# Kernel tuning notes

Hardware: AMD Instinct MI355X
Metric: run time of the kernel (lower is better)

Reference implementation:

```python
import jax, jax.numpy as jnp
import numpy as np

Q_DIM = 32
HID = 512
OFF = Q_DIM * (Q_DIM - 1) // 2  # 496 strictly-lower-triangular entries


def setup_inputs() -> dict:
    key = jax.random.key(0)
    ks = jax.random.split(key, 20)

    def w(k, shape, fan_in):
        return (jax.random.normal(k, shape, jnp.float32) / np.float32(np.sqrt(fan_in)))

    return {
        "q": jax.random.normal(ks[0], (1, Q_DIM), jnp.float32),
        "q_t": jax.random.normal(ks[1], (1, Q_DIM), jnp.float32),
        "q_tt": jax.random.normal(ks[2], (1, Q_DIM), jnp.float32),
        # L-network (torch Linear convention: y = x @ W.T + b)
        "W1": w(ks[3], (HID, Q_DIM), Q_DIM), "b1": jnp.zeros((HID,), jnp.float32),
        "W2": w(ks[4], (HID, HID), HID),     "b2": jnp.zeros((HID,), jnp.float32),
        "W3": w(ks[5], (HID, HID), HID),     "b3": jnp.zeros((HID,), jnp.float32),
        "Wd": w(ks[6], (Q_DIM, HID), HID),   "bd": jnp.zeros((Q_DIM,), jnp.float32),
        "Wo": w(ks[7], (OFF, HID), HID),     "bo": jnp.zeros((OFF,), jnp.float32),
        # g-network
        "Wg1": w(ks[8], (HID, Q_DIM), Q_DIM), "bg1": jnp.zeros((HID,), jnp.float32),
        "Wg2": w(ks[9], (HID, HID), HID),     "bg2": jnp.zeros((HID,), jnp.float32),
        "Wg3": w(ks[10], (Q_DIM, HID), HID),  "bg3": jnp.zeros((Q_DIM,), jnp.float32),
    }


def reference(q, q_t, q_tt, W1, b1, W2, b2, W3, b3, Wd, bd, Wo, bo,
              Wg1, bg1, Wg2, bg2, Wg3, bg3):
    n = Q_DIM
    # L-network forward (sigmoid MLP)
    h1 = jax.nn.sigmoid(q @ W1.T + b1)    # [1, 512]
    h2 = jax.nn.sigmoid(h1 @ W2.T + b2)   # [1, 512]
    h3 = jax.nn.sigmoid(h2 @ W3.T + b3)   # [1, 512]
    l_diag = jnp.exp(h3 @ Wd.T + bd)      # [1, n]
    l_off = h3 @ Wo.T + bo                # [1, OFF]

    # Assemble lower-triangular L. The torch loop fills the strictly-lower
    # triangle in row-major order: (1,0),(2,0),(2,1),(3,0),... == tril_indices(k=-1).
    rows, cols = jnp.tril_indices(n, -1)
    ar = jnp.arange(n)
    L = (jnp.zeros((n, n), q.dtype)
         .at[ar, ar].set(l_diag[0])
         .at[rows, cols].set(l_off[0]))

    # Analytic Jacobian chain. diag_embed(s) @ W == s[:,None] * W (row scaling).
    s1 = (h1 * (1.0 - h1))[0]             # sigmoid'
    s2 = (h2 * (1.0 - h2))[0]
    s3 = (h3 * (1.0 - h3))[0]
    dh1 = s1[:, None] * W1                # [512, n]
    dh2 = s2[:, None] * W2                # [512, 512]
    dh3 = s3[:, None] * W3                # [512, 512]
    dh4 = jnp.concatenate([l_diag[0][:, None] * Wd, Wo], axis=0)  # [n+OFF, 512]
    dl_dq = dh4 @ (dh3 @ (dh2 @ dh1))     # [n+OFF, n]

    # dL_dq[i, j, k] = d L[i,j] / d q_k  (same tril assembly, vectorized over k)
    dL_dq = (jnp.zeros((n, n, n), q.dtype)
             .at[ar, ar, :].set(dl_dq[:n])
             .at[rows, cols, :].set(dl_dq[n:]))

    qt_col = q_t.T                        # [n, 1]
    Dqt = jnp.einsum('ijk,k->ij', dL_dq, q_t[0])   # comp_3_1 / squeeze pattern
    Fjk = jnp.einsum('ijk,i->jk', dL_dq, q_t[0])   # comp_4_1 pattern
    LTqt = L.T @ qt_col                   # [n, 1]

    comp_1 = L @ (L.T @ q_tt.T)
    comp_2 = L @ (Dqt.T @ qt_col)
    comp_3 = Dqt @ LTqt
    comp_4 = Fjk @ LTqt
    comp_5 = (q_t @ (L @ Dqt.T)).T

    # g-network
    g1 = jax.nn.sigmoid(q @ Wg1.T + bg1)
    g2 = jax.nn.sigmoid(g1 @ Wg2.T + bg2)
    g = (g2 @ Wg3.T + bg3).reshape(n, 1)

    tau = comp_1 + comp_2 + comp_3 - 0.5 * comp_4 - 0.5 * comp_5 + g
    return tau.T                          # [1, n]
```

## Files before the change

kernel.cpp:

```cpp
#include <hip/hip_runtime.h>
#include <cmath>

#define NQ 32
#define H 512
#define NOFF 496
#define NR4 528
#define NC 33

__device__ __forceinline__ float sigmoidf(float x) {
    return 1.0f / (1.0f + __expf(-x));
}

__global__ void __launch_bounds__(512) k1(const float* __restrict__ q,
                   const float* __restrict__ W1, const float* __restrict__ b1,
                   const float* __restrict__ Wg1, const float* __restrict__ bg1,
                   float* __restrict__ h1, float* __restrict__ A_cm,
                   float* __restrict__ g1) {
    __shared__ float qs[NQ];
    int j = threadIdx.x;
    if (j < NQ) qs[j] = q[j];
    __syncthreads();
    const float* w1r = W1 + j * NQ;
    const float* wg1r = Wg1 + j * NQ;
    float acc = 0.f, accg = 0.f;
    #pragma unroll
    for (int k = 0; k < NQ; ++k) {
        acc  += w1r[k]  * qs[k];
        accg += wg1r[k] * qs[k];
    }
    float h = sigmoidf(acc + b1[j]);
    h1[j] = h;
    float s = h * (1.f - h);
    #pragma unroll
    for (int k = 0; k < NQ; ++k)
        A_cm[k * H + j] = s * w1r[k];
    g1[j] = sigmoidf(accg + bg1[j]);
}

__global__ void __launch_bounds__(256) k2(const float* __restrict__ W2, const float* __restrict__ Wg2,
                   const float* __restrict__ h1, const float* __restrict__ A_cm,
                   const float* __restrict__ g1,
                   float* __restrict__ Y, float* __restrict__ g2pre) {
    int k = blockIdx.x;
    int rb = blockIdx.y;
    int lane = threadIdx.x & 63;
    int wv = threadIdx.x >> 6;
    const float* B; const float* M; float* out;
    if (k == 0)      { B = h1;               M = W2;  out = Y; }
    else if (k < NC) { B = A_cm + (k-1) * H; M = W2;  out = Y + k * H; }
    else             { B = g1;               M = Wg2; out = g2pre; }
    float breg[8];
    #pragma unroll
    for (int t = 0; t < 8; ++t) breg[t] = B[lane + (t << 6)];
    int r0 = rb * 64 + wv * 16;
    #pragma unroll 4
    for (int i = 0; i < 16; ++i) {
        int r = r0 + i;
        const float* wr = M + (size_t)r * H;
        float acc = 0.f;
        #pragma unroll
        for (int t = 0; t < 8; ++t) acc += wr[lane + (t << 6)] * breg[t];
        #pragma unroll
        for (int m = 32; m > 0; m >>= 1) acc += __shfl_xor(acc, m, 64);
        if (lane == 0) out[r] = acc;
    }
}

__global__ void __launch_bounds__(256) k3(const float* __restrict__ W3, const float* __restrict__ Wg3,
                   const float* __restrict__ Y, const float* __restrict__ b2,
                   const float* __restrict__ g2pre, const float* __restrict__ bg2,
                   const float* __restrict__ bg3,
                   float* __restrict__ Z, float* __restrict__ gvec) {
    int k = blockIdx.x;
    int rb = blockIdx.y;
    int lane = threadIdx.x & 63;
    int wv = threadIdx.x >> 6;
    if (k == NC) {
        if (rb != 0) return;
        float breg[8];
        #pragma unroll
        for (int t = 0; t < 8; ++t) {
            int j = lane + (t << 6);
            breg[t] = sigmoidf(g2pre[j] + bg2[j]);
        }
        #pragma unroll
        for (int i = 0; i < 8; ++i) {
            int r = wv * 8 + i;
            const float* wr = Wg3 + (size_t)r * H;
            float acc = 0.f;
            #pragma unroll
            for (int t = 0; t < 8; ++t) acc += wr[lane + (t << 6)] * breg[t];
            #pragma unroll
            for (int m = 32; m > 0; m >>= 1) acc += __shfl_xor(acc, m, 64);
            if (lane == 0) gvec[r] = acc + bg3[r];
        }
        return;
    }
    float breg[8];
    #pragma unroll
    for (int t = 0; t < 8; ++t) {
        int j = lane + (t << 6);
        float h2 = sigmoidf(Y[j] + b2[j]);
        breg[t] = (k == 0) ? h2 : h2 * (1.f - h2) * Y[k * H + j];
    }
    float* out = Z + k * H;
    int r0 = rb * 64 + wv * 16;
    #pragma unroll 4
    for (int i = 0; i < 16; ++i) {
        int r = r0 + i;
        const float* wr = W3 + (size_t)r * H;
        float acc = 0.f;
        #pragma unroll
        for (int t = 0; t < 8; ++t) acc += wr[lane + (t << 6)] * breg[t];
        #pragma unroll
        for (int m = 32; m > 0; m >>= 1) acc += __shfl_xor(acc, m, 64);
        if (lane == 0) out[r] = acc;
    }
}

__global__ void __launch_bounds__(256) k4(const float* __restrict__ Wd, const float* __restrict__ Wo,
                   const float* __restrict__ Z, const float* __restrict__ b3,
                   float* __restrict__ U) {
    int k = blockIdx.x;
    int rb = blockIdx.y;
    int lane = threadIdx.x & 63;
    int wv = threadIdx.x >> 6;
    float breg[8];
    #pragma unroll
    for (int t = 0; t < 8; ++t) {
        int j = lane + (t << 6);
        float h3 = sigmoidf(Z[j] + b3[j]);
        breg[t] = (k == 0) ? h3 : h3 * (1.f - h3) * Z[k * H + j];
    }
    int r0 = rb * 64 + wv * 16;
    for (int i = 0; i < 16; ++i) {
        int r = r0 + i;
        if (r >= NR4) break;
        const float* wr = (r < NQ) ? (Wd + (size_t)r * H) : (Wo + (size_t)(r - NQ) * H);
        float acc = 0.f;
        #pragma unroll
        for (int t = 0; t < 8; ++t) acc += wr[lane + (t << 6)] * breg[t];
        #pragma unroll
        for (int m = 32; m > 0; m >>= 1) acc += __shfl_xor(acc, m, 64);
        if (lane == 0) U[k * NR4 + r] = acc;
    }
}

__global__ void __launch_bounds__(256) k5(const float* __restrict__ U,
                   const float* __restrict__ bd, const float* __restrict__ bo,
                   const float* __restrict__ q_t, const float* __restrict__ q_tt,
                   const float* __restrict__ gvec,
                   float* __restrict__ out) {
    __shared__ float ldiag[NQ], loff[NOFF], vv[NR4];
    __shared__ float Lm[NQ][NQ + 1], Dq[NQ][NQ + 1], Fj[NQ][NQ + 1];
    __shared__ float qts[NQ], qtts[NQ], LTq[NQ], t1[NQ], u2[NQ];
    int tid = threadIdx.x;
    if (tid < NQ) {
        ldiag[tid] = __expf(U[tid] + bd[tid]);
        qts[tid]  = q_t[tid];
        qtts[tid] = q_tt[tid];
    }
    for (int r = tid; r < NOFF; r += 256)
        loff[r] = U[NQ + r] + bo[r];
    __syncthreads();
    for (int m = tid; m < NR4; m += 256) {
        float acc = 0.f;
        #pragma unroll
        for (int kk = 0; kk < NQ; ++kk)
            acc += U[(kk + 1) * NR4 + m] * qts[kk];
        vv[m] = (m < NQ) ? ldiag[m] * acc : acc;
    }
    for (int p = tid; p < NQ * NQ; p += 256) {
        int i = p >> 5, j = p & 31;
        Lm[i][j] = (i == j) ? ldiag[i]
                 : (j < i ? loff[i * (i - 1) / 2 + j] : 0.f);
    }
    for (int p = tid; p < NQ * NQ; p += 256) {
        int j = p >> 5, k = p & 31;
        const float* Uc = U + (k + 1) * NR4;
        float acc = qts[j] * ldiag[j] * Uc[j];
        for (int i = j + 1; i < NQ; ++i)
            acc += qts[i] * Uc[NQ + i * (i - 1) / 2 + j];
        Fj[j][k] = acc;
    }
    __syncthreads();
    for (int p = tid; p < NQ * NQ; p += 256) {
        int i = p >> 5, j = p & 31;
        Dq[i][j] = (i == j) ? vv[i]
                 : (j < i ? vv[NQ + i * (i - 1) / 2 + j] : 0.f);
    }
    if (tid < NQ) {
        int kcol = tid;
        float a = 0.f, b = 0.f;
        #pragma unroll
        for (int j = 0; j < NQ; ++j) {
            a += Lm[j][kcol] * qts[j];
            b += Lm[j][kcol] * qtts[j];
        }
        LTq[kcol] = a;
        t1[kcol] = b;
    }
    __syncthreads();
    if (tid < NQ) {
        int kcol = tid;
        float a = 0.f;
        #pragma unroll
        for (int j = 0; j < NQ; ++j) a += Dq[j][kcol] * qts[j];
        u2[kcol] = a;
    }
    __syncthreads();
    if (tid < NQ) {
        int i = tid;
        float c1 = 0.f, c2 = 0.f, c3 = 0.f, c4 = 0.f;
        #pragma unroll
        for (int kk = 0; kk < NQ; ++kk) {
            c1 += Lm[i][kk] * t1[kk];
            c2 += Lm[i][kk] * u2[kk];
            c3 += Dq[i][kk] * LTq[kk];
            c4 += Fj[i][kk] * LTq[kk];
        }
        out[i] = c1 + c2 + 0.5f * c3 - 0.5f * c4 + gvec[i];
    }
}

extern "C" void kernel_launch(void* const* d_in, const int* in_sizes, int n_in,
                              void* d_out, int out_size, void* d_ws, size_t ws_size,
                              hipStream_t stream) {
    const float* q    = (const float*)d_in[0];
    const float* q_t  = (const float*)d_in[1];
    const float* q_tt = (const float*)d_in[2];
    const float* W1   = (const float*)d_in[3];
    const float* b1   = (const float*)d_in[4];
    const float* W2   = (const float*)d_in[5];
    const float* b2   = (const float*)d_in[6];
    const float* W3   = (const float*)d_in[7];
    const float* b3   = (const float*)d_in[8];
    const float* Wd   = (const float*)d_in[9];
    const float* bd   = (const float*)d_in[10];
    const float* Wo   = (const float*)d_in[11];
    const float* bo   = (const float*)d_in[12];
    const float* Wg1  = (const float*)d_in[13];
    const float* bg1  = (const float*)d_in[14];
    const float* Wg2  = (const float*)d_in[15];
    const float* bg2  = (const float*)d_in[16];
    const float* Wg3  = (const float*)d_in[17];
    const float* bg3  = (const float*)d_in[18];

    float* ws = (float*)d_ws;
    float* h1    = ws;
    float* A_cm  = ws + 512;
    float* g1    = ws + 16896;
    float* Y     = ws + 17408;
    float* g2pre = ws + 34304;
    float* Z     = ws + 34816;
    float* gvec  = ws + 51712;
    float* U     = ws + 51744;
    float* out   = (float*)d_out;

    hipLaunchKernelGGL(k1, dim3(1), dim3(512), 0, stream,
                       q, W1, b1, Wg1, bg1, h1, A_cm, g1);
    hipLaunchKernelGGL(k2, dim3(34, 8), dim3(256), 0, stream,
                       W2, Wg2, h1, A_cm, g1, Y, g2pre);
    hipLaunchKernelGGL(k3, dim3(34, 8), dim3(256), 0, stream,
                       W3, Wg3, Y, b2, g2pre, bg2, bg3, Z, gvec);
    hipLaunchKernelGGL(k4, dim3(33, 9), dim3(256), 0, stream,
                       Wd, Wo, Z, b3, U);
    hipLaunchKernelGGL(k5, dim3(1), dim3(256), 0, stream,
                       U, bd, bo, q_t, q_tt, gvec, out);
}
```

Measured before the change: 156.9 us.

## Fuse five kernels into one cooperative kernel with grid syncs and float4 loads

Replaces the five separate launches with a single cooperative kernel of 297 blocks that uses grid.sync between the layer stages. The first-layer work (h1, the scaled W1 column, g1) is recomputed redundantly inside each stage-2 block, which removes k1 and its workspace buffers. Matrix-vector inner loops now use float4 loads. The goal is to cut launch overhead and inter-kernel gaps. In exchange it adds grid-wide barrier cost and per-block redundant first-layer compute, and the final small stage still runs on one block while the others wait.

```diff
diff --git a/kernel.cpp b/kernel.cpp
--- a/kernel.cpp
+++ b/kernel.cpp
@@ -1,5 +1,8 @@
 #include <hip/hip_runtime.h>
+#include <hip/hip_cooperative_groups.h>
 #include <cmath>
+
+namespace cg = cooperative_groups;
 
 #define NQ 32
 #define H 512
@@ -10,216 +13,229 @@
 __device__ __forceinline__ float sigmoidf(float x) {
     return 1.0f / (1.0f + __expf(-x));
 }
-
-__global__ void __launch_bounds__(512) k1(const float* __restrict__ q,
-                   const float* __restrict__ W1, const float* __restrict__ b1,
-                   const float* __restrict__ Wg1, const float* __restrict__ bg1,
-                   float* __restrict__ h1, float* __restrict__ A_cm,
-                   float* __restrict__ g1) {
+__device__ __forceinline__ float dot4(float4 a, float4 b) {
+    return a.x * b.x + a.y * b.y + a.z * b.z + a.w * b.w;
+}
+__device__ __forceinline__ float4 sig4(float4 a) {
+    return make_float4(sigmoidf(a.x), sigmoidf(a.y), sigmoidf(a.z), sigmoidf(a.w));
+}
+
+__global__ void __launch_bounds__(256, 2) fused(
+    const float* __restrict__ q, const float* __restrict__ q_t, const float* __restrict__ q_tt,
+    const float* __restrict__ W1, const float* __restrict__ b1,
+    const float* __restrict__ W2, const float* __restrict__ b2,
+    const float* __restrict__ W3, const float* __restrict__ b3,
+    const float* __restrict__ Wd, const float* __restrict__ bd,
+    const float* __restrict__ Wo, const float* __restrict__ bo,
+    const float* __restrict__ Wg1, const float* __restrict__ bg1,
+    const float* __restrict__ Wg2, const float* __restrict__ bg2,
+    const float* __restrict__ Wg3, const float* __restrict__ bg3,
+    float* __restrict__ Y, float* __restrict__ g2pre,
+    float* __restrict__ Z, float* __restrict__ gvec,
+    float* __restrict__ U, float* __restrict__ out)
+{
+    cg::grid_group grid = cg::this_grid();
+    const int b = blockIdx.x;
+    const int tid = threadIdx.x;
+    const int lane = tid & 63, wv = tid >> 6;
+
     __shared__ float qs[NQ];
-    int j = threadIdx.x;
-    if (j < NQ) qs[j] = q[j];
-    __syncthreads();
-    const float* w1r = W1 + j * NQ;
-    const float* wg1r = Wg1 + j * NQ;
-    float acc = 0.f, accg = 0.f;
-    #pragma unroll
-    for (int k = 0; k < NQ; ++k) {
-        acc  += w1r[k]  * qs[k];
-        accg += wg1r[k] * qs[k];
-    }
-    float h = sigmoidf(acc + b1[j]);
-    h1[j] = h;
-    float s = h * (1.f - h);
-    #pragma unroll
-    for (int k = 0; k < NQ; ++k)
-        A_cm[k * H + j] = s * w1r[k];
-    g1[j] = sigmoidf(accg + bg1[j]);
-}
-
-__global__ void __launch_bounds__(256) k2(const float* __restrict__ W2, const float* __restrict__ Wg2,
-                   const float* __restrict__ h1, const float* __restrict__ A_cm,
-                   const float* __restrict__ g1,
-                   float* __restrict__ Y, float* __restrict__ g2pre) {
-    int k = blockIdx.x;
-    int rb = blockIdx.y;
-    int lane = threadIdx.x & 63;
-    int wv = threadIdx.x >> 6;
-    const float* B; const float* M; float* out;
-    if (k == 0)      { B = h1;               M = W2;  out = Y; }
-    else if (k < NC) { B = A_cm + (k-1) * H; M = W2;  out = Y + k * H; }
-    else             { B = g1;               M = Wg2; out = g2pre; }
-    float breg[8];
-    #pragma unroll
-    for (int t = 0; t < 8; ++t) breg[t] = B[lane + (t << 6)];
-    int r0 = rb * 64 + wv * 16;
-    #pragma unroll 4
-    for (int i = 0; i < 16; ++i) {
-        int r = r0 + i;
-        const float* wr = M + (size_t)r * H;
-        float acc = 0.f;
-        #pragma unroll
-        for (int t = 0; t < 8; ++t) acc += wr[lane + (t << 6)] * breg[t];
-        #pragma unroll
-        for (int m = 32; m > 0; m >>= 1) acc += __shfl_xor(acc, m, 64);
-        if (lane == 0) out[r] = acc;
-    }
-}
-
-__global__ void __launch_bounds__(256) k3(const float* __restrict__ W3, const float* __restrict__ Wg3,
-                   const float* __restrict__ Y, const float* __restrict__ b2,
-                   const float* __restrict__ g2pre, const float* __restrict__ bg2,
-                   const float* __restrict__ bg3,
-                   float* __restrict__ Z, float* __restrict__ gvec) {
-    int k = blockIdx.x;
-    int rb = blockIdx.y;
-    int lane = threadIdx.x & 63;
-    int wv = threadIdx.x >> 6;
-    if (k == NC) {
-        if (rb != 0) return;
-        float breg[8];
-        #pragma unroll
-        for (int t = 0; t < 8; ++t) {
-            int j = lane + (t << 6);
-            breg[t] = sigmoidf(g2pre[j] + bg2[j]);
-        }
-        #pragma unroll
-        for (int i = 0; i < 8; ++i) {
-            int r = wv * 8 + i;
-            const float* wr = Wg3 + (size_t)r * H;
-            float acc = 0.f;
-            #pragma unroll
-            for (int t = 0; t < 8; ++t) acc += wr[lane + (t << 6)] * breg[t];
-            #pragma unroll
-            for (int m = 32; m > 0; m >>= 1) acc += __shfl_xor(acc, m, 64);
-            if (lane == 0) gvec[r] = acc + bg3[r];
-        }
-        return;
-    }
-    float breg[8];
-    #pragma unroll
-    for (int t = 0; t < 8; ++t) {
-        int j = lane + (t << 6);
-        float h2 = sigmoidf(Y[j] + b2[j]);
-        breg[t] = (k == 0) ? h2 : h2 * (1.f - h2) * Y[k * H + j];
-    }
-    float* out = Z + k * H;
-    int r0 = rb * 64 + wv * 16;
-    #pragma unroll 4
-    for (int i = 0; i < 16; ++i) {
-        int r = r0 + i;
-        const float* wr = W3 + (size_t)r * H;
-        float acc = 0.f;
-        #pragma unroll
-        for (int t = 0; t < 8; ++t) acc += wr[lane + (t << 6)] * breg[t];
-        #pragma unroll
-        for (int m = 32; m > 0; m >>= 1) acc += __shfl_xor(acc, m, 64);
-        if (lane == 0) out[r] = acc;
-    }
-}
-
-__global__ void __launch_bounds__(256) k4(const float* __restrict__ Wd, const float* __restrict__ Wo,
-                   const float* __restrict__ Z, const float* __restrict__ b3,
-                   float* __restrict__ U) {
-    int k = blockIdx.x;
-    int rb = blockIdx.y;
-    int lane = threadIdx.x & 63;
-    int wv = threadIdx.x >> 6;
-    float breg[8];
-    #pragma unroll
-    for (int t = 0; t < 8; ++t) {
-        int j = lane + (t << 6);
-        float h3 = sigmoidf(Z[j] + b3[j]);
-        breg[t] = (k == 0) ? h3 : h3 * (1.f - h3) * Z[k * H + j];
-    }
-    int r0 = rb * 64 + wv * 16;
-    for (int i = 0; i < 16; ++i) {
-        int r = r0 + i;
-        if (r >= NR4) break;
-        const float* wr = (r < NQ) ? (Wd + (size_t)r * H) : (Wo + (size_t)(r - NQ) * H);
-        float acc = 0.f;
-        #pragma unroll
-        for (int t = 0; t < 8; ++t) acc += wr[lane + (t << 6)] * breg[t];
-        #pragma unroll
-        for (int m = 32; m > 0; m >>= 1) acc += __shfl_xor(acc, m, 64);
-        if (lane == 0) U[k * NR4 + r] = acc;
-    }
-}
-
-__global__ void __launch_bounds__(256) k5(const float* __restrict__ U,
-                   const float* __restrict__ bd, const float* __restrict__ bo,
-                   const float* __restrict__ q_t, const float* __restrict__ q_tt,
-                   const float* __restrict__ gvec,
-                   float* __restrict__ out) {
     __shared__ float ldiag[NQ], loff[NOFF], vv[NR4];
     __shared__ float Lm[NQ][NQ + 1], Dq[NQ][NQ + 1], Fj[NQ][NQ + 1];
-    __shared__ float qts[NQ], qtts[NQ], LTq[NQ], t1[NQ], u2[NQ];
-    int tid = threadIdx.x;
-    if (tid < NQ) {
-        ldiag[tid] = __expf(U[tid] + bd[tid]);
-        qts[tid]  = q_t[tid];
-        qtts[tid] = q_tt[tid];
-    }
-    for (int r = tid; r < NOFF; r += 256)
-        loff[r] = U[NQ + r] + bo[r];
+    __shared__ float qts[NQ], qtts[NQ], LTq[NQ], t1s[NQ], u2[NQ];
+
+    if (tid < NQ) qs[tid] = q[tid];
     __syncthreads();
-    for (int m = tid; m < NR4; m += 256) {
-        float acc = 0.f;
+
+    if (b < 272) {
+        const int k = b >> 3, rb = b & 7;
+        const float* Wf = (k == NC) ? Wg1 : W1;
+        const float* bf = (k == NC) ? bg1 : b1;
+        float4 breg[2];
         #pragma unroll
-        for (int kk = 0; kk < NQ; ++kk)
-            acc += U[(kk + 1) * NR4 + m] * qts[kk];
-        vv[m] = (m < NQ) ? ldiag[m] * acc : acc;
-    }
-    for (int p = tid; p < NQ * NQ; p += 256) {
-        int i = p >> 5, j = p & 31;
-        Lm[i][j] = (i == j) ? ldiag[i]
-                 : (j < i ? loff[i * (i - 1) / 2 + j] : 0.f);
-    }
-    for (int p = tid; p < NQ * NQ; p += 256) {
-        int j = p >> 5, k = p & 31;
-        const float* Uc = U + (k + 1) * NR4;
-        float acc = qts[j] * ldiag[j] * Uc[j];
-        for (int i = j + 1; i < NQ; ++i)
-            acc += qts[i] * Uc[NQ + i * (i - 1) / 2 + j];
-        Fj[j][k] = acc;
-    }
-    __syncthreads();
-    for (int p = tid; p < NQ * NQ; p += 256) {
-        int i = p >> 5, j = p & 31;
-        Dq[i][j] = (i == j) ? vv[i]
-                 : (j < i ? vv[NQ + i * (i - 1) / 2 + j] : 0.f);
-    }
-    if (tid < NQ) {
-        int kcol = tid;
-        float a = 0.f, b = 0.f;
+        for (int t = 0; t < 2; ++t) {
+            float rr[4];
+            #pragma unroll
+            for (int u = 0; u < 4; ++u) {
+                int j = 4 * (lane + t * 64) + u;
+                const float4* w = (const float4*)(Wf + j * NQ);
+                float acc = 0.f;
+                #pragma unroll
+                for (int c = 0; c < 8; ++c) {
+                    float4 wc = w[c];
+                    acc += wc.x * qs[4*c] + wc.y * qs[4*c+1] + wc.z * qs[4*c+2] + wc.w * qs[4*c+3];
+                }
+                float h = sigmoidf(acc + bf[j]);
+                rr[u] = (k == 0 || k == NC) ? h : h * (1.f - h) * Wf[j * NQ + (k - 1)];
+            }
+            breg[t] = make_float4(rr[0], rr[1], rr[2], rr[3]);
+        }
+        const float4* Mv = (const float4*)((k == NC) ? Wg2 : W2);
+        float* outp = (k == NC) ? g2pre : (Y + k * H);
+        int r0 = rb * 64 + wv * 16;
+        #pragma unroll 4
+        for (int i = 0; i < 16; ++i) {
+            int r = r0 + i;
+            const float4* wr = Mv + (size_t)r * (H / 4);
+            float acc = dot4(wr[lane], breg[0]) + dot4(wr[lane + 64], breg[1]);
+            #pragma unroll
+            for (int m = 32; m > 0; m >>= 1) acc += __shfl_xor(acc, m, 64);
+            if (lane == 0) outp[r] = acc;
+        }
+    }
+    grid.sync();
+
+    if (b < 272) {
+        const int k = b >> 3, rb = b & 7;
+        if (k == NC) {
+            if (rb == 0) {
+                const float4* Gp = (const float4*)g2pre;
+                const float4* Bg = (const float4*)bg2;
+                float4 breg[2];
+                #pragma unroll
+                for (int t = 0; t < 2; ++t) {
+                    float4 a = Gp[lane + t * 64], bb = Bg[lane + t * 64];
+                    breg[t] = sig4(make_float4(a.x + bb.x, a.y + bb.y, a.z + bb.z, a.w + bb.w));
+                }
+                #pragma unroll
+                for (int i = 0; i < 8; ++i) {
+                    int r = wv * 8 + i;
+                    const float4* wr = (const float4*)Wg3 + (size_t)r * (H / 4);
+                    float acc = dot4(wr[lane], breg[0]) + dot4(wr[lane + 64], breg[1]);
+                    #pragma unroll
+                    for (int m = 32; m > 0; m >>= 1) acc += __shfl_xor(acc, m, 64);
+                    if (lane == 0) gvec[r] = acc + bg3[r];
+                }
+            }
+        } else {
+            const float4* Y0 = (const float4*)Y;
+            const float4* Yk = (const float4*)(Y + k * H);
+            const float4* B2 = (const float4*)b2;
+            float4 breg[2];
+            #pragma unroll
+            for (int t = 0; t < 2; ++t) {
+                float4 y0 = Y0[lane + t * 64], bb = B2[lane + t * 64];
+                float4 h = sig4(make_float4(y0.x + bb.x, y0.y + bb.y, y0.z + bb.z, y0.w + bb.w));
+                if (k == 0) breg[t] = h;
+                else {
+                    float4 yk = Yk[lane + t * 64];
+                    breg[t] = make_float4(h.x * (1.f - h.x) * yk.x, h.y * (1.f - h.y) * yk.y,
+                                          h.z * (1.f - h.z) * yk.z, h.w * (1.f - h.w) * yk.w);
+                }
+            }
+            float* outp = Z + k * H;
+            int r0 = rb * 64 + wv * 16;
+            #pragma unroll 4
+            for (int i = 0; i < 16; ++i) {
+                int r = r0 + i;
+                const float4* wr = (const float4*)W3 + (size_t)r * (H / 4);
+                float acc = dot4(wr[lane], breg[0]) + dot4(wr[lane + 64], breg[1]);
+                #pragma unroll
+                for (int m = 32; m > 0; m >>= 1) acc += __shfl_xor(acc, m, 64);
+                if (lane == 0) outp[r] = acc;
+            }
+        }
+    }
+    grid.sync();
+
+    {
+        const int k = b / 9, rb = b % 9;
+        const float4* Z0 = (const float4*)Z;
+        const float4* Zk = (const float4*)(Z + k * H);
+        const float4* B3 = (const float4*)b3;
+        float4 breg[2];
         #pragma unroll
-        for (int j = 0; j < NQ; ++j) {
-            a += Lm[j][kcol] * qts[j];
-            b += Lm[j][kcol] * qtts[j];
-        }
-        LTq[kcol] = a;
-        t1[kcol] = b;
-    }
-    __syncthreads();
-    if (tid < NQ) {
-        int kcol = tid;
-        float a = 0.f;
-        #pragma unroll
-        for (int j = 0; j < NQ; ++j) a += Dq[j][kcol] * qts[j];
-        u2[kcol] = a;
-    }
-    __syncthreads();
-    if (tid < NQ) {
-        int i = tid;
-        float c1 = 0.f, c2 = 0.f, c3 = 0.f, c4 = 0.f;
-        #pragma unroll
-        for (int kk = 0; kk < NQ; ++kk) {
-            c1 += Lm[i][kk] * t1[kk];
-            c2 += Lm[i][kk] * u2[kk];
-            c3 += Dq[i][kk] * LTq[kk];
-            c4 += Fj[i][kk] * LTq[kk];
-        }
-        out[i] = c1 + c2 + 0.5f * c3 - 0.5f * c4 + gvec[i];
+        for (int t = 0; t < 2; ++t) {
+            float4 z0 = Z0[lane + t * 64], bb = B3[lane + t * 64];
+            float4 h = sig4(make_float4(z0.x + bb.x, z0.y + bb.y, z0.z + bb.z, z0.w + bb.w));
+            if (k == 0) breg[t] = h;
+            else {
+                float4 zk = Zk[lane + t * 64];
+                breg[t] = make_float4(h.x * (1.f - h.x) * zk.x, h.y * (1.f - h.y) * zk.y,
+                                      h.z * (1.f - h.z) * zk.z, h.w * (1.f - h.w) * zk.w);
+            }
+        }
+        int r0 = rb * 64 + wv * 16;
+        for (int i = 0; i < 16; ++i) {
+            int r = r0 + i;
+            if (r >= NR4) break;
+            const float4* wr = (r < NQ) ? ((const float4*)Wd + (size_t)r * (H / 4))
+                                        : ((const float4*)Wo + (size_t)(r - NQ) * (H / 4));
+            float acc = dot4(wr[lane], breg[0]) + dot4(wr[lane + 64], breg[1]);
+            #pragma unroll
+            for (int m = 32; m > 0; m >>= 1) acc += __shfl_xor(acc, m, 64);
+            if (lane == 0) U[k * NR4 + r] = acc;
+        }
+    }
+    grid.sync();
+
+    if (b == 0) {
+        if (tid < NQ) {
+            ldiag[tid] = __expf(U[tid] + bd[tid]);
+            qts[tid]  = q_t[tid];
+            qtts[tid] = q_tt[tid];
+        }
+        for (int r = tid; r < NOFF; r += 256)
+            loff[r] = U[NQ + r] + bo[r];
+        __syncthreads();
+        for (int m = tid; m < NR4; m += 256) {
+            float acc = 0.f;
+            #pragma unroll
+            for (int kk = 0; kk < NQ; ++kk)
+                acc += U[(kk + 1) * NR4 + m] * qts[kk];
+            vv[m] = (m < NQ) ? ldiag[m] * acc : acc;
+        }
+        for (int p = tid; p < NQ * NQ; p += 256) {
+            int i = p >> 5, j = p & 31;
+            Lm[i][j] = (i == j) ? ldiag[i]
+                     : (j < i ? loff[i * (i - 1) / 2 + j] : 0.f);
+        }
+        for (int p = tid; p < NQ * NQ; p += 256) {
+            int j = p >> 5, k = p & 31;
+            const float* Uc = U + (k + 1) * NR4;
+            float acc = qts[j] * ldiag[j] * Uc[j];
+            for (int i = j + 1; i < NQ; ++i)
+                acc += qts[i] * Uc[NQ + i * (i - 1) / 2 + j];
+            Fj[j][k] = acc;
+        }
+        __syncthreads();
+        for (int p = tid; p < NQ * NQ; p += 256) {
+            int i = p >> 5, j = p & 31;
+            Dq[i][j] = (i == j) ? vv[i]
+                     : (j < i ? vv[NQ + i * (i - 1) / 2 + j] : 0.f);
+        }
+        if (tid < NQ) {
+            int kcol = tid;
+            float a = 0.f, bsum = 0.f;
+            #pragma unroll
+            for (int j = 0; j < NQ; ++j) {
+                a    += Lm[j][kcol] * qts[j];
+                bsum += Lm[j][kcol] * qtts[j];
+            }
+            LTq[kcol] = a;
+            t1s[kcol] = bsum;
+        }
+        __syncthreads();
+        if (tid < NQ) {
+            int kcol = tid;
+            float a = 0.f;
+            #pragma unroll
+            for (int j = 0; j < NQ; ++j) a += Dq[j][kcol] * qts[j];
+            u2[kcol] = a;
+        }
+        __syncthreads();
+        if (tid < NQ) {
+            int i = tid;
+            float c1 = 0.f, c2 = 0.f, c3 = 0.f, c4 = 0.f;
+            #pragma unroll
+            for (int kk = 0; kk < NQ; ++kk) {
+                c1 += Lm[i][kk] * t1s[kk];
+                c2 += Lm[i][kk] * u2[kk];
+                c3 += Dq[i][kk] * LTq[kk];
+                c4 += Fj[i][kk] * LTq[kk];
+            }
+            out[i] = c1 + c2 + 0.5f * c3 - 0.5f * c4 + gvec[i];
+        }
     }
 }
 
@@ -247,24 +263,19 @@
     const float* bg3  = (const float*)d_in[18];
 
     float* ws = (float*)d_ws;
-    float* h1    = ws;
-    float* A_cm  = ws + 512;
-    float* g1    = ws + 16896;
-    float* Y     = ws + 17408;
-    float* g2pre = ws + 34304;
-    float* Z     = ws + 34816;
-    float* gvec  = ws + 51712;
-    float* U     = ws + 51744;
+    float* Y     = ws;
+    float* g2pre = ws + 16896;
+    float* Z     = ws + 17408;
+    float* gvec  = ws + 34304;
+    float* U     = ws + 34336;
     float* out   = (float*)d_out;
 
-    hipLaunchKernelGGL(k1, dim3(1), dim3(512), 0, stream,
-                       q, W1, b1, Wg1, bg1, h1, A_cm, g1);
-    hipLaunchKernelGGL(k2, dim3(34, 8), dim3(256), 0, stream,
-                       W2, Wg2, h1, A_cm, g1, Y, g2pre);
-    hipLaunchKernelGGL(k3, dim3(34, 8), dim3(256), 0, stream,
-                       W3, Wg3, Y, b2, g2pre, bg2, bg3, Z, gvec);
-    hipLaunchKernelGGL(k4, dim3(33, 9), dim3(256), 0, stream,
-                       Wd, Wo, Z, b3, U);
-    hipLaunchKernelGGL(k5, dim3(1), dim3(256), 0, stream,
-                       U, bd, bo, q_t, q_tt, gvec, out);
-}
+    void* args[] = {
+        (void*)&q, (void*)&q_t, (void*)&q_tt,
+        (void*)&W1, (void*)&b1, (void*)&W2, (void*)&b2, (void*)&W3, (void*)&b3,
+        (void*)&Wd, (void*)&bd, (void*)&Wo, (void*)&bo,
+        (void*)&Wg1, (void*)&bg1, (void*)&Wg2, (void*)&bg2, (void*)&Wg3, (void*)&bg3,
+        (void*)&Y, (void*)&g2pre, (void*)&Z, (void*)&gvec, (void*)&U, (void*)&out
+    };
+    hipLaunchCooperativeKernel((void*)fused, dim3(297), dim3(256), args, 0, stream);
+}
```

Measured after the change: 269.6 us. 1.72x slower.
